# Optimization experiments

Hardware: AMD Instinct MI355X
Metric: run time of the kernel (lower is better)

The kernel has to match this reference:

```python
import jax, jax.numpy as jnp
import numpy as np

N_LEVELS = 16
BASE_RES = 16.0
MAX_RES = 128.0
LOG2_T = 19
T_SIZE = 2 ** LOG2_T
F = 2

# primes wrapped to int32 to mimic torch int32 overflow semantics
P0 = np.int32(1)
P1 = np.int32(np.uint32(2654435761))
P2 = np.int32(np.uint32(805459861))

# corner offsets matching (c_000,c_100,c_010,c_001,c_110,c_101,c_011,c_111)
OFFSETS = np.array([[0,0,0],[1,0,0],[0,1,0],[0,0,1],
                    [1,1,0],[1,0,1],[0,1,1],[1,1,1]], dtype=np.int32)


def setup_inputs() -> dict:
    key = jax.random.key(0)
    k1, k2 = jax.random.split(key)
    x = jax.random.uniform(k1, (1048576, 3), dtype=jnp.float32)
    hashtable = jax.random.uniform(k2, (T_SIZE, F), dtype=jnp.float32) * 2.0 - 1.0
    return {"x": x, "hashtable": hashtable}


def _resolutions():
    growth = np.exp((np.log(MAX_RES) - np.log(BASE_RES)) / (N_LEVELS - 1))
    return np.floor(BASE_RES * growth ** np.arange(N_LEVELS)).astype(np.float32)  # [L]


def reference(x, hashtable):
    res = jnp.asarray(_resolutions())                      # [L]
    xs = x[None, :, :] * res[:, None, None]                # [L,N,3]
    xf = jnp.floor(xs)
    xfi = xf.astype(jnp.int32)                             # [L,N,3]
    xci = jnp.ceil(xs).astype(jnp.int32)                   # [L,N,3]
    d = xs - xf                                            # [L,N,3] interp weights

    off = jnp.asarray(OFFSETS)[:, None, None, :]           # [8,1,1,3]
    corners = jnp.where(off == 1, xci[None], xfi[None])    # [8,L,N,3]

    h = (corners[..., 0] * P0) ^ (corners[..., 1] * P1) ^ (corners[..., 2] * P2)
    h = jnp.mod(h, T_SIZE)                                 # [8,L,N], nonnegative

    v = hashtable[h]                                       # [8,L,N,F]

    w = jnp.where(off == 1, d[None], 1.0 - d[None])        # [8,L,N,3]
    w = jnp.prod(w, axis=-1)                               # [8,L,N]

    enc = jnp.sum(v * w[..., None], axis=0)                # [L,N,F]
    N = x.shape[0]
    return jnp.transpose(enc, (1, 0, 2)).reshape(N, N_LEVELS * F)
```

## Files before the change

kernel.cpp:

```cpp
#include <hip/hip_runtime.h>


__constant__ float c_res[16] = {
    16.f, 18.f, 21.f, 24.f, 27.f, 32.f, 36.f, 42.f,
    48.f, 55.f, 64.f, 73.f, 84.f, 97.f, 111.f, 128.f
};

#define TMASK   0x7FFFFu
#define PRIME1  2654435761u
#define PRIME2  805459861u
#define NBUCKET 4096
#define CACHE_N 4467

__device__ __forceinline__ int bucket_of(float x0, float x1, float x2) {
    int c0 = (int)(x0 * 16.f); c0 = c0 < 0 ? 0 : (c0 > 15 ? 15 : c0);
    int c1 = (int)(x1 * 16.f); c1 = c1 < 0 ? 0 : (c1 > 15 ? 15 : c1);
    int c2 = (int)(x2 * 16.f); c2 = c2 < 0 ? 0 : (c2 > 15 ? 15 : c2);
    return (c0 << 8) | (c1 << 4) | c2;
}


__global__ __launch_bounds__(256)
void k_hist(const float* __restrict__ x, unsigned* __restrict__ cnt, int npts) {
    __shared__ unsigned h[NBUCKET];
    for (int i = threadIdx.x; i < NBUCKET; i += 256) h[i] = 0u;
    __syncthreads();
    int nb = gridDim.x;
    int chunk = (npts + nb - 1) / nb;
    int begin = blockIdx.x * chunk;
    int end   = begin + chunk; if (end > npts) end = npts;
    for (int i = begin + threadIdx.x; i < end; i += 256) {
        int b = bucket_of(x[3 * i], x[3 * i + 1], x[3 * i + 2]);
        atomicAdd(&h[b], 1u);
    }
    __syncthreads();
    for (int i = threadIdx.x; i < NBUCKET; i += 256)
        cnt[blockIdx.x * NBUCKET + i] = h[i];
}

template<int NBT>
__global__ __launch_bounds__(256)
void k_colscan(const unsigned* __restrict__ cnt, unsigned* __restrict__ base,
               unsigned* __restrict__ colsum) {
    const int RPG = NBT / 8;
    int col = blockIdx.x * 32 + (threadIdx.x & 31);
    int rg  = threadIdx.x >> 5;
    unsigned loc[RPG];
    unsigned s = 0;
    #pragma unroll
    for (int r = 0; r < RPG; ++r) {
        unsigned v = cnt[(size_t)(rg * RPG + r) * NBUCKET + col];
        loc[r] = s;
        s += v;
    }
    __shared__ unsigned t[8][32];
    t[rg][threadIdx.x & 31] = s;
    __syncthreads();
    unsigned pre = 0;
    for (int g = 0; g < rg; ++g) pre += t[g][threadIdx.x & 31];
    #pragma unroll
    for (int r = 0; r < RPG; ++r)
        base[(size_t)(rg * RPG + r) * NBUCKET + col] = pre + loc[r];
    if (rg == 7) colsum[col] = pre + s;
}

__global__ __launch_bounds__(1024)
void k_scan(const unsigned* __restrict__ colsum, unsigned* __restrict__ starts) {
    __shared__ unsigned tmp[1024];
    int t = threadIdx.x;
    unsigned v0 = colsum[4 * t + 0], v1 = colsum[4 * t + 1];
    unsigned v2 = colsum[4 * t + 2], v3 = colsum[4 * t + 3];
    unsigned s = v0 + v1 + v2 + v3;
    tmp[t] = s;
    __syncthreads();
    for (int off = 1; off < 1024; off <<= 1) {
        unsigned u = (t >= off) ? tmp[t - off] : 0u;
        __syncthreads();
        tmp[t] += u;
        __syncthreads();
    }
    unsigned excl = tmp[t] - s;
    starts[4 * t + 0] = excl;
    starts[4 * t + 1] = excl + v0;
    starts[4 * t + 2] = excl + v0 + v1;
    starts[4 * t + 3] = excl + v0 + v1 + v2;
    if (t == 1023) starts[4096] = tmp[1023];
}

template<int MODE>
__global__ __launch_bounds__(256)
void k_scatter(const float* __restrict__ x, const unsigned* __restrict__ base,
               const unsigned* __restrict__ starts, unsigned* __restrict__ perm,
               float4* __restrict__ xs, int npts) {
    __shared__ unsigned cur[NBUCKET];
    for (int i = threadIdx.x; i < NBUCKET; i += 256)
        cur[i] = starts[i] + base[blockIdx.x * NBUCKET + i];
    __syncthreads();
    int nb = gridDim.x;
    int chunk = (npts + nb - 1) / nb;
    int begin = blockIdx.x * chunk;
    int end   = begin + chunk; if (end > npts) end = npts;
    for (int i = begin + threadIdx.x; i < end; i += 256) {
        float x0 = x[3 * i], x1 = x[3 * i + 1], x2 = x[3 * i + 2];
        int b = bucket_of(x0, x1, x2);
        unsigned pos = atomicAdd(&cur[b], 1u);
        if constexpr (MODE == 0) {
            float4 v; v.x = x0; v.y = x1; v.z = x2;
            v.w = __uint_as_float((unsigned)i);
            xs[pos] = v;
        } else {
            perm[pos] = (unsigned)i;
        }
    }
}


template<int MODE>
__global__ __launch_bounds__(256)
void k_main(const float4* __restrict__ xs, const float* __restrict__ x,
            const unsigned* __restrict__ perm,
            const unsigned* __restrict__ starts, const float2* __restrict__ tab,
            float4* __restrict__ out4)
{
    __shared__ float2 cache[CACHE_N];
    __shared__ int4 metaA[16];
    __shared__ int4 metaB[16];

    int cell = blockIdx.x;
    int startp = starts[cell], endp = starts[cell + 1];
    if (startp == endp) return;

    int ci = (cell >> 8) & 15, cj = (cell >> 4) & 15, ck = cell & 15;
    float fi0 = ci * 0.0625f, fi1 = (ci + 1) * 0.0625f;
    float fj0 = cj * 0.0625f, fj1 = (cj + 1) * 0.0625f;
    float fk0 = ck * 0.0625f, fk1 = (ck + 1) * 0.0625f;

    int cbase = 0;
    #pragma unroll 1
    for (int l = 0; l < 16; ++l) {
        float r = c_res[l];
        int lo0 = (int)floorf(fi0 * r), hi0 = (int)ceilf(fi1 * r);
        int lo1 = (int)floorf(fj0 * r), hi1 = (int)ceilf(fj1 * r);
        int lo2 = (int)floorf(fk0 * r), hi2 = (int)ceilf(fk1 * r);
        int n0 = hi0 - lo0 + 1, n1 = hi1 - lo1 + 1, n2 = hi2 - lo2 + 1;
        int n12 = n1 * n2, tot = n0 * n12;
        for (int t = threadIdx.x; t < tot; t += 256) {
            int a = t / n12, rem = t - a * n12;
            int b = rem / n2, d = rem - b * n2;
            unsigned h = ((unsigned)(lo0 + a)
                        ^ ((unsigned)(lo1 + b) * PRIME1)
                        ^ ((unsigned)(lo2 + d) * PRIME2)) & TMASK;
            cache[cbase + t] = tab[h];
        }
        if (threadIdx.x == 0) {
            metaA[l] = make_int4(lo0, lo1, lo2, cbase);
            metaB[l] = make_int4(n12, n2, __float_as_int(r), 0);
        }
        cbase += tot;
    }
    __syncthreads();

    auto lvl = [&](int l, float a0, float a1, float a2, float& ex, float& ey) {
        int4 mA = metaA[l];
        int4 mB = metaB[l];
        float r = __int_as_float(mB.z);
        int n12 = mB.x, n2 = mB.y;
        float s0 = a0 * r, s1 = a1 * r, s2 = a2 * r;
        float f0 = floorf(s0), f1 = floorf(s1), f2 = floorf(s2);
        float d0 = s0 - f0, d1 = s1 - f1, d2 = s2 - f2;
        int A0 = (int)f0 - mA.x, A1 = (int)f1 - mA.y, A2 = (int)f2 - mA.z;
        int e0 = (d0 != 0.f) ? n12 : 0;
        int e1 = (d1 != 0.f) ? n2  : 0;
        int e2 = (d2 != 0.f) ? 1   : 0;
        int rA = mA.w + A0 * n12 + A1 * n2 + A2;

        float2 v0 = cache[rA];
        float2 v1 = cache[rA + e0];
        float2 v2 = cache[rA + e1];
        float2 v3 = cache[rA + e2];
        float2 v4 = cache[rA + e0 + e1];
        float2 v5 = cache[rA + e0 + e2];
        float2 v6 = cache[rA + e1 + e2];
        float2 v7 = cache[rA + e0 + e1 + e2];

        float u0 = 1.f - d0, u1 = 1.f - d1, u2 = 1.f - d2;
        float pa = u1 * u2, pb = d1 * u2, pc = u1 * d2, pe = d1 * d2;
        float w0 = u0 * pa, w1 = d0 * pa, w2 = u0 * pb, w3 = u0 * pc;
        float w4 = d0 * pb, w5 = d0 * pc, w6 = u0 * pe, w7 = d0 * pe;

        float rx = v0.x * w0, ry = v0.y * w0;
        rx += v1.x * w1;  ry += v1.y * w1;
        rx += v2.x * w2;  ry += v2.y * w2;
        rx += v3.x * w3;  ry += v3.y * w3;
        rx += v4.x * w4;  ry += v4.y * w4;
        rx += v5.x * w5;  ry += v5.y * w5;
        rx += v6.x * w6;  ry += v6.y * w6;
        rx += v7.x * w7;  ry += v7.y * w7;
        ex = rx; ey = ry;
    };

    auto fetch = [&](int s, float& a0, float& a1, float& a2, unsigned& pp) {
        if constexpr (MODE == 0) {
            float4 v = xs[s];
            a0 = v.x; a1 = v.y; a2 = v.z; pp = __float_as_uint(v.w);
        } else {
            pp = perm[s];
            a0 = x[3 * pp]; a1 = x[3 * pp + 1]; a2 = x[3 * pp + 2];
        }
    };

    int sp = startp + (int)threadIdx.x;
    if (sp >= endp) return;
    float x0, x1, x2; unsigned p;
    fetch(sp, x0, x1, x2, p);
    while (true) {
        int spn = sp + 256;
        bool more = spn < endp;
        float nx0, nx1, nx2; unsigned np;
        if (more) fetch(spn, nx0, nx1, nx2, np);

        #pragma unroll 1
        for (int lp = 0; lp < 8; ++lp) {
            float4 o;
            lvl(2 * lp,     x0, x1, x2, o.x, o.y);
            lvl(2 * lp + 1, x0, x1, x2, o.z, o.w);
            out4[(size_t)p * 8 + lp] = o;
        }

        if (!more) break;
        x0 = nx0; x1 = nx1; x2 = nx2; p = np;
        sp = spn;
    }
}

__global__ __launch_bounds__(256, 8)
void k_fallback(const float* __restrict__ x, const float2* __restrict__ tab,
                float2* __restrict__ out, int total) {
    int tid = blockIdx.x * 256 + threadIdx.x;
    if (tid >= total) return;
    int p = tid >> 4, l = tid & 15;
    float r = c_res[l];
    float s0 = x[3*p] * r, s1 = x[3*p+1] * r, s2 = x[3*p+2] * r;
    float f0 = floorf(s0), f1 = floorf(s1), f2 = floorf(s2);
    float d0 = s0 - f0, d1 = s1 - f1, d2 = s2 - f2;
    unsigned A0 = (unsigned)(int)f0, B0 = (unsigned)(int)ceilf(s0);
    unsigned A1 = (unsigned)(int)f1 * PRIME1, B1 = (unsigned)(int)ceilf(s1) * PRIME1;
    unsigned A2 = (unsigned)(int)f2 * PRIME2, B2 = (unsigned)(int)ceilf(s2) * PRIME2;
    unsigned h0=(A0^A1^A2)&TMASK, h1=(B0^A1^A2)&TMASK, h2=(A0^B1^A2)&TMASK;
    unsigned h3=(A0^A1^B2)&TMASK, h4=(B0^B1^A2)&TMASK, h5=(B0^A1^B2)&TMASK;
    unsigned h6=(A0^B1^B2)&TMASK, h7=(B0^B1^B2)&TMASK;
    float2 v0=tab[h0],v1=tab[h1],v2=tab[h2],v3=tab[h3];
    float2 v4=tab[h4],v5=tab[h5],v6=tab[h6],v7=tab[h7];
    float u0=1.f-d0,u1=1.f-d1,u2=1.f-d2;
    float ex = v0.x*(u0*u1*u2), ey = v0.y*(u0*u1*u2);
    ex += v1.x*(d0*u1*u2); ey += v1.y*(d0*u1*u2);
    ex += v2.x*(u0*d1*u2); ey += v2.y*(u0*d1*u2);
    ex += v3.x*(u0*u1*d2); ey += v3.y*(u0*u1*d2);
    ex += v4.x*(d0*d1*u2); ey += v4.y*(d0*d1*u2);
    ex += v5.x*(d0*u1*d2); ey += v5.y*(d0*u1*d2);
    ex += v6.x*(u0*d1*d2); ey += v6.y*(u0*d1*d2);
    ex += v7.x*(d0*d1*d2); ey += v7.y*(d0*d1*d2);
    float2 o; o.x = ex; o.y = ey; out[tid] = o;
}

extern "C" void kernel_launch(void* const* d_in, const int* in_sizes, int n_in,
                              void* d_out, int out_size, void* d_ws, size_t ws_size,
                              hipStream_t stream)
{
    const float*  x   = (const float*)d_in[0];
    const float2* tab = (const float2*)d_in[1];
    int npts = in_sizes[0] / 3;

    {
        const int NBA = 256;
        size_t off_cnt    = 0;
        size_t off_base   = off_cnt    + (size_t)NBA * NBUCKET * 4;
        size_t off_colsum = off_base   + (size_t)NBA * NBUCKET * 4;
        size_t off_starts = off_colsum + (size_t)NBUCKET * 4;
        size_t off_xs     = (off_starts + (size_t)(NBUCKET + 1) * 4 + 63)
                            & ~(size_t)63;
        size_t need       = off_xs + (size_t)npts * 16;
        if (ws_size >= need) {
            unsigned* cnt    = (unsigned*)((char*)d_ws + off_cnt);
            unsigned* base   = (unsigned*)((char*)d_ws + off_base);
            unsigned* colsum = (unsigned*)((char*)d_ws + off_colsum);
            unsigned* starts = (unsigned*)((char*)d_ws + off_starts);
            float4*   xs     = (float4*)  ((char*)d_ws + off_xs);

            k_hist        <<<NBA, 256, 0, stream>>>(x, cnt, npts);
            k_colscan<256><<<NBUCKET / 32, 256, 0, stream>>>(cnt, base, colsum);
            k_scan        <<<1, 1024, 0, stream>>>(colsum, starts);
            k_scatter<0>  <<<NBA, 256, 0, stream>>>(x, base, starts,
                                                    nullptr, xs, npts);
            k_main<0>     <<<NBUCKET, 256, 0, stream>>>(xs, x, nullptr, starts,
                                                        tab, (float4*)d_out);
            return;
        }
    }

    {
        const int NBB = 128;
        size_t off_cnt    = 0;
        size_t off_base   = off_cnt    + (size_t)NBB * NBUCKET * 4;
        size_t off_colsum = off_base   + (size_t)NBB * NBUCKET * 4;
        size_t off_starts = off_colsum + (size_t)NBUCKET * 4;
        size_t off_perm   = (off_starts + (size_t)(NBUCKET + 1) * 4 + 63)
                            & ~(size_t)63;
        size_t need       = off_perm + (size_t)npts * 4;
        if (ws_size >= need) {
            unsigned* cnt    = (unsigned*)((char*)d_ws + off_cnt);
            unsigned* base   = (unsigned*)((char*)d_ws + off_base);
            unsigned* colsum = (unsigned*)((char*)d_ws + off_colsum);
            unsigned* starts = (unsigned*)((char*)d_ws + off_starts);
            unsigned* perm   = (unsigned*)((char*)d_ws + off_perm);

            k_hist        <<<NBB, 256, 0, stream>>>(x, cnt, npts);
            k_colscan<128><<<NBUCKET / 32, 256, 0, stream>>>(cnt, base, colsum);
            k_scan        <<<1, 1024, 0, stream>>>(colsum, starts);
            k_scatter<1>  <<<NBB, 256, 0, stream>>>(x, base, starts,
                                                    perm, nullptr, npts);
            k_main<1>     <<<NBUCKET, 256, 0, stream>>>(nullptr, x, perm, starts,
                                                        tab, (float4*)d_out);
            return;
        }
    }

    int total = npts * 16;
    k_fallback<<<(total + 255) / 256, 256, 0, stream>>>(
        x, tab, (float2*)d_out, total);
}
```

Baseline: 257.9 us.

## Fuse binning passes into cooperative kernel and phase the per-cell table cache

Replaces the four binning kernels (histogram, column scan, scan, scatter) with one cooperative kernel that uses grid syncs and keeps each block's point chunk in LDS, so it reads x once and saves launches. The main kernel now fills its shared-memory corner cache in three level phases (14-15, 10-13, 0-9) instead of all 16 levels at once. This shrinks LDS from about 35KB to 14KB and adds a launch bound of 8 blocks per SM to raise occupancy. In exchange each point is re-read from xs three times, and there are extra barriers plus a fallback path if the cooperative launch fails.

Result: slower. 611.9 us (+137.3%).

```diff
diff --git a/kernel.cpp b/kernel.cpp
--- a/kernel.cpp
+++ b/kernel.cpp
@@ -1,4 +1,7 @@
 #include <hip/hip_runtime.h>
+#include <hip/hip_cooperative_groups.h>
+
+namespace cg = cooperative_groups;
 
 
 __constant__ float c_res[16] = {
@@ -10,13 +13,115 @@
 #define PRIME1  2654435761u
 #define PRIME2  805459861u
 #define NBUCKET 4096
-#define CACHE_N 4467
+#define CACHE_PH 1800
 
 __device__ __forceinline__ int bucket_of(float x0, float x1, float x2) {
     int c0 = (int)(x0 * 16.f); c0 = c0 < 0 ? 0 : (c0 > 15 ? 15 : c0);
     int c1 = (int)(x1 * 16.f); c1 = c1 < 0 ? 0 : (c1 > 15 ? 15 : c1);
     int c2 = (int)(x2 * 16.f); c2 = c2 < 0 ? 0 : (c2 > 15 ? 15 : c2);
     return (c0 << 8) | (c1 << 4) | c2;
+}
+
+__global__ __launch_bounds__(1024)
+void k_sort(const float* __restrict__ x, unsigned* __restrict__ cnt,
+            unsigned* __restrict__ base, unsigned* __restrict__ colsum,
+            unsigned* __restrict__ starts, float4* __restrict__ xs, int npts)
+{
+    extern __shared__ char smem[];
+    float*    xraw = (float*)smem;
+    unsigned* cur  = (unsigned*)(smem + 49152);
+    unsigned* tbl  = (unsigned*)(smem + 49152 + 16384);
+
+    const int tid = threadIdx.x;
+    const int blk = blockIdx.x;
+    const int chunk = npts >> 8;
+    const int begin = blk * chunk;
+
+    {
+        const float4* src = (const float4*)(x + (size_t)begin * 3);
+        float4* dst = (float4*)xraw;
+        const int nf4 = (chunk * 3) >> 2;
+        for (int i = tid; i < nf4; i += 1024) dst[i] = src[i];
+    }
+    for (int j = tid; j < NBUCKET; j += 1024) cur[j] = 0u;
+    __syncthreads();
+    for (int i = tid; i < chunk; i += 1024) {
+        int b = bucket_of(xraw[3*i], xraw[3*i+1], xraw[3*i+2]);
+        atomicAdd(&cur[b], 1u);
+    }
+    __syncthreads();
+    for (int j = tid; j < NBUCKET; j += 1024)
+        cnt[(size_t)blk * NBUCKET + j] = cur[j];
+
+    __threadfence();
+    cg::this_grid().sync();
+
+    {
+        int c = tid & 15, g = tid >> 4;
+        int col = blk * 16 + c;
+        unsigned loc[4], s = 0;
+        #pragma unroll
+        for (int k = 0; k < 4; ++k) {
+            unsigned v = cnt[(size_t)(g * 4 + k) * NBUCKET + col];
+            loc[k] = s; s += v;
+        }
+        tbl[g * 16 + c] = s;
+        __syncthreads();
+        for (int off = 1; off < 64; off <<= 1) {
+            unsigned u = (g >= off) ? tbl[(g - off) * 16 + c] : 0u;
+            __syncthreads();
+            tbl[g * 16 + c] += u;
+            __syncthreads();
+        }
+        unsigned pre = tbl[g * 16 + c] - s;
+        #pragma unroll
+        for (int k = 0; k < 4; ++k)
+            base[(size_t)(g * 4 + k) * NBUCKET + col] = pre + loc[k];
+        if (g == 63) colsum[col] = pre + s;
+    }
+
+    __threadfence();
+    cg::this_grid().sync();
+
+    {
+        unsigned v0 = colsum[4*tid+0], v1 = colsum[4*tid+1];
+        unsigned v2 = colsum[4*tid+2], v3 = colsum[4*tid+3];
+        unsigned s = v0 + v1 + v2 + v3;
+        tbl[tid] = s;
+        __syncthreads();
+        for (int off = 1; off < 1024; off <<= 1) {
+            unsigned u = (tid >= off) ? tbl[tid - off] : 0u;
+            __syncthreads();
+            tbl[tid] += u;
+            __syncthreads();
+        }
+        unsigned excl = tbl[tid] - s;
+        unsigned b0 = base[(size_t)blk * NBUCKET + 4*tid + 0];
+        unsigned b1 = base[(size_t)blk * NBUCKET + 4*tid + 1];
+        unsigned b2 = base[(size_t)blk * NBUCKET + 4*tid + 2];
+        unsigned b3 = base[(size_t)blk * NBUCKET + 4*tid + 3];
+        cur[4*tid+0] = excl + b0;
+        cur[4*tid+1] = excl + v0 + b1;
+        cur[4*tid+2] = excl + v0 + v1 + b2;
+        cur[4*tid+3] = excl + v0 + v1 + v2 + b3;
+        if (blk == 0) {
+            starts[4*tid+0] = excl;
+            starts[4*tid+1] = excl + v0;
+            starts[4*tid+2] = excl + v0 + v1;
+            starts[4*tid+3] = excl + v0 + v1 + v2;
+            if (tid == 1023) starts[NBUCKET] = tbl[1023];
+        }
+    }
+    __syncthreads();
+
+    for (int i = tid; i < chunk; i += 1024) {
+        float x0 = xraw[3*i], x1 = xraw[3*i+1], x2 = xraw[3*i+2];
+        int b = bucket_of(x0, x1, x2);
+        unsigned pos = atomicAdd(&cur[b], 1u);
+        float4 v; v.x = x0; v.y = x1; v.z = x2;
+        v.w = __uint_as_float((unsigned)(begin + i));
+        xs[pos] = v;
+    }
 }
 
 
@@ -116,13 +221,13 @@
 
 
 template<int MODE>
-__global__ __launch_bounds__(256)
+__global__ __launch_bounds__(256, 8)
 void k_main(const float4* __restrict__ xs, const float* __restrict__ x,
             const unsigned* __restrict__ perm,
             const unsigned* __restrict__ starts, const float2* __restrict__ tab,
             float4* __restrict__ out4)
 {
-    __shared__ float2 cache[CACHE_N];
+    __shared__ float2 cache[CACHE_PH];
     __shared__ int4 metaA[16];
     __shared__ int4 metaB[16];
 
@@ -134,31 +239,6 @@
     float fi0 = ci * 0.0625f, fi1 = (ci + 1) * 0.0625f;
     float fj0 = cj * 0.0625f, fj1 = (cj + 1) * 0.0625f;
     float fk0 = ck * 0.0625f, fk1 = (ck + 1) * 0.0625f;
-
-    int cbase = 0;
-    #pragma unroll 1
-    for (int l = 0; l < 16; ++l) {
-        float r = c_res[l];
-        int lo0 = (int)floorf(fi0 * r), hi0 = (int)ceilf(fi1 * r);
-        int lo1 = (int)floorf(fj0 * r), hi1 = (int)ceilf(fj1 * r);
-        int lo2 = (int)floorf(fk0 * r), hi2 = (int)ceilf(fk1 * r);
-        int n0 = hi0 - lo0 + 1, n1 = hi1 - lo1 + 1, n2 = hi2 - lo2 + 1;
-        int n12 = n1 * n2, tot = n0 * n12;
-        for (int t = threadIdx.x; t < tot; t += 256) {
-            int a = t / n12, rem = t - a * n12;
-            int b = rem / n2, d = rem - b * n2;
-            unsigned h = ((unsigned)(lo0 + a)
-                        ^ ((unsigned)(lo1 + b) * PRIME1)
-                        ^ ((unsigned)(lo2 + d) * PRIME2)) & TMASK;
-            cache[cbase + t] = tab[h];
-        }
-        if (threadIdx.x == 0) {
-            metaA[l] = make_int4(lo0, lo1, lo2, cbase);
-            metaB[l] = make_int4(n12, n2, __float_as_int(r), 0);
-        }
-        cbase += tot;
-    }
-    __syncthreads();
 
     auto lvl = [&](int l, float a0, float a1, float a2, float& ex, float& ey) {
         int4 mA = metaA[l];
@@ -199,37 +279,54 @@
         ex = rx; ey = ry;
     };
 
-    auto fetch = [&](int s, float& a0, float& a1, float& a2, unsigned& pp) {
-        if constexpr (MODE == 0) {
-            float4 v = xs[s];
-            a0 = v.x; a1 = v.y; a2 = v.z; pp = __float_as_uint(v.w);
-        } else {
-            pp = perm[s];
-            a0 = x[3 * pp]; a1 = x[3 * pp + 1]; a2 = x[3 * pp + 2];
-        }
-    };
-
-    int sp = startp + (int)threadIdx.x;
-    if (sp >= endp) return;
-    float x0, x1, x2; unsigned p;
-    fetch(sp, x0, x1, x2, p);
-    while (true) {
-        int spn = sp + 256;
-        bool more = spn < endp;
-        float nx0, nx1, nx2; unsigned np;
-        if (more) fetch(spn, nx0, nx1, nx2, np);
-
+    #pragma unroll
+    for (int ph = 0; ph < 3; ++ph) {
+        const int llo = (ph == 0) ? 14 : (ph == 1) ? 10 : 0;
+        const int lhi = (ph == 0) ? 16 : (ph == 1) ? 14 : 10;
+
+        int cbase = 0;
         #pragma unroll 1
-        for (int lp = 0; lp < 8; ++lp) {
-            float4 o;
-            lvl(2 * lp,     x0, x1, x2, o.x, o.y);
-            lvl(2 * lp + 1, x0, x1, x2, o.z, o.w);
-            out4[(size_t)p * 8 + lp] = o;
-        }
-
-        if (!more) break;
-        x0 = nx0; x1 = nx1; x2 = nx2; p = np;
-        sp = spn;
+        for (int l = llo; l < lhi; ++l) {
+            float r = c_res[l];
+            int lo0 = (int)floorf(fi0 * r), hi0 = (int)ceilf(fi1 * r);
+            int lo1 = (int)floorf(fj0 * r), hi1 = (int)ceilf(fj1 * r);
+            int lo2 = (int)floorf(fk0 * r), hi2 = (int)ceilf(fk1 * r);
+            int n0 = hi0 - lo0 + 1, n1 = hi1 - lo1 + 1, n2 = hi2 - lo2 + 1;
+            int n12 = n1 * n2, tot = n0 * n12;
+            for (int t = threadIdx.x; t < tot; t += 256) {
+                int a = t / n12, rem = t - a * n12;
+                int b = rem / n2, d = rem - b * n2;
+                unsigned h = ((unsigned)(lo0 + a)
+                            ^ ((unsigned)(lo1 + b) * PRIME1)
+                            ^ ((unsigned)(lo2 + d) * PRIME2)) & TMASK;
+                cache[cbase + t] = tab[h];
+            }
+            if (threadIdx.x == 0) {
+                metaA[l] = make_int4(lo0, lo1, lo2, cbase);
+                metaB[l] = make_int4(n12, n2, __float_as_int(r), 0);
+            }
+            cbase += tot;
+        }
+        __syncthreads();
+
+        for (int sp = startp + (int)threadIdx.x; sp < endp; sp += 256) {
+            float x0, x1, x2; unsigned p;
+            if constexpr (MODE == 0) {
+                float4 v = xs[sp];
+                x0 = v.x; x1 = v.y; x2 = v.z; p = __float_as_uint(v.w);
+            } else {
+                p = perm[sp];
+                x0 = x[3 * p]; x1 = x[3 * p + 1]; x2 = x[3 * p + 2];
+            }
+            #pragma unroll 1
+            for (int lp = (llo >> 1); lp < (lhi >> 1); ++lp) {
+                float4 o;
+                lvl(2 * lp,     x0, x1, x2, o.x, o.y);
+                lvl(2 * lp + 1, x0, x1, x2, o.z, o.w);
+                out4[(size_t)p * 8 + lp] = o;
+            }
+        }
+        __syncthreads();
     }
 }
 
@@ -287,11 +384,24 @@
             unsigned* starts = (unsigned*)((char*)d_ws + off_starts);
             float4*   xs     = (float4*)  ((char*)d_ws + off_xs);
 
-            k_hist        <<<NBA, 256, 0, stream>>>(x, cnt, npts);
-            k_colscan<256><<<NBUCKET / 32, 256, 0, stream>>>(cnt, base, colsum);
-            k_scan        <<<1, 1024, 0, stream>>>(colsum, starts);
-            k_scatter<0>  <<<NBA, 256, 0, stream>>>(x, base, starts,
-                                                    nullptr, xs, npts);
+            bool coop_ok = false;
+            if ((npts % 1024) == 0 && (npts >> 8) <= 4096) {
+                int np = npts;
+                void* args[] = { (void*)&x, (void*)&cnt, (void*)&base,
+                                 (void*)&colsum, (void*)&starts, (void*)&xs,
+                                 (void*)&np };
+                unsigned shmem = 49152u + 16384u + 4096u;
+                hipError_t e = hipLaunchCooperativeKernel(
+                    (void*)k_sort, dim3(256), dim3(1024), args, shmem, stream);
+                coop_ok = (e == hipSuccess);
+            }
+            if (!coop_ok) {
+                k_hist        <<<NBA, 256, 0, stream>>>(x, cnt, npts);
+                k_colscan<256><<<NBUCKET / 32, 256, 0, stream>>>(cnt, base, colsum);
+                k_scan        <<<1, 1024, 0, stream>>>(colsum, starts);
+                k_scatter<0>  <<<NBA, 256, 0, stream>>>(x, base, starts,
+                                                        nullptr, xs, npts);
+            }
             k_main<0>     <<<NBUCKET, 256, 0, stream>>>(xs, x, nullptr, starts,
                                                         tab, (float4*)d_out);
             return;
```

## Replace per-block count/colscan sort with global atomic histogram and cursors

Applied to the files above, without the earlier changes.

The binning pipeline drops the per-block count matrix and column-scan kernel. It now uses a global histogram built with shared atomics then global atomic merges, a single scan that also initialises global cursors, and a scatter using global atomics on those cursors. The main kernel moves to 512 threads per block with an 8-block occupancy hint and drops the software prefetch of the next point. This cuts launches and the workspace traffic of the count and base matrices, but adds heavy global-atomic contention in the scatter and makes the sort order nondeterministic.

Result: slower. 311.0 us (+20.6%).

```diff
diff --git a/kernel.cpp b/kernel.cpp
--- a/kernel.cpp
+++ b/kernel.cpp
@@ -19,57 +19,30 @@
     return (c0 << 8) | (c1 << 4) | c2;
 }
 
-
 __global__ __launch_bounds__(256)
-void k_hist(const float* __restrict__ x, unsigned* __restrict__ cnt, int npts) {
+void k_hist(const float* __restrict__ x, unsigned* __restrict__ hist, int npts) {
     __shared__ unsigned h[NBUCKET];
-    for (int i = threadIdx.x; i < NBUCKET; i += 256) h[i] = 0u;
-    __syncthreads();
-    int nb = gridDim.x;
-    int chunk = (npts + nb - 1) / nb;
-    int begin = blockIdx.x * chunk;
-    int end   = begin + chunk; if (end > npts) end = npts;
-    for (int i = begin + threadIdx.x; i < end; i += 256) {
+    for (int j = threadIdx.x; j < NBUCKET; j += 256) h[j] = 0u;
+    __syncthreads();
+    int stride = gridDim.x * 256;
+    for (int i = blockIdx.x * 256 + threadIdx.x; i < npts; i += stride) {
         int b = bucket_of(x[3 * i], x[3 * i + 1], x[3 * i + 2]);
         atomicAdd(&h[b], 1u);
     }
     __syncthreads();
-    for (int i = threadIdx.x; i < NBUCKET; i += 256)
-        cnt[blockIdx.x * NBUCKET + i] = h[i];
-}
-
-template<int NBT>
-__global__ __launch_bounds__(256)
-void k_colscan(const unsigned* __restrict__ cnt, unsigned* __restrict__ base,
-               unsigned* __restrict__ colsum) {
-    const int RPG = NBT / 8;
-    int col = blockIdx.x * 32 + (threadIdx.x & 31);
-    int rg  = threadIdx.x >> 5;
-    unsigned loc[RPG];
-    unsigned s = 0;
-    #pragma unroll
-    for (int r = 0; r < RPG; ++r) {
-        unsigned v = cnt[(size_t)(rg * RPG + r) * NBUCKET + col];
-        loc[r] = s;
-        s += v;
-    }
-    __shared__ unsigned t[8][32];
-    t[rg][threadIdx.x & 31] = s;
-    __syncthreads();
-    unsigned pre = 0;
-    for (int g = 0; g < rg; ++g) pre += t[g][threadIdx.x & 31];
-    #pragma unroll
-    for (int r = 0; r < RPG; ++r)
-        base[(size_t)(rg * RPG + r) * NBUCKET + col] = pre + loc[r];
-    if (rg == 7) colsum[col] = pre + s;
+    for (int j = threadIdx.x; j < NBUCKET; j += 256) {
+        unsigned v = h[j];
+        if (v) atomicAdd(&hist[j], v);
+    }
 }
 
 __global__ __launch_bounds__(1024)
-void k_scan(const unsigned* __restrict__ colsum, unsigned* __restrict__ starts) {
+void k_scan(const unsigned* __restrict__ hist, unsigned* __restrict__ starts,
+            unsigned* __restrict__ cursor) {
     __shared__ unsigned tmp[1024];
     int t = threadIdx.x;
-    unsigned v0 = colsum[4 * t + 0], v1 = colsum[4 * t + 1];
-    unsigned v2 = colsum[4 * t + 2], v3 = colsum[4 * t + 3];
+    unsigned v0 = hist[4 * t + 0], v1 = hist[4 * t + 1];
+    unsigned v2 = hist[4 * t + 2], v3 = hist[4 * t + 3];
     unsigned s = v0 + v1 + v2 + v3;
     tmp[t] = s;
     __syncthreads();
@@ -80,30 +53,23 @@
         __syncthreads();
     }
     unsigned excl = tmp[t] - s;
-    starts[4 * t + 0] = excl;
-    starts[4 * t + 1] = excl + v0;
-    starts[4 * t + 2] = excl + v0 + v1;
-    starts[4 * t + 3] = excl + v0 + v1 + v2;
-    if (t == 1023) starts[4096] = tmp[1023];
+    unsigned s1 = excl + v0, s2 = s1 + v1, s3 = s2 + v2;
+    starts[4 * t + 0] = excl;  cursor[4 * t + 0] = excl;
+    starts[4 * t + 1] = s1;    cursor[4 * t + 1] = s1;
+    starts[4 * t + 2] = s2;    cursor[4 * t + 2] = s2;
+    starts[4 * t + 3] = s3;    cursor[4 * t + 3] = s3;
+    if (t == 1023) starts[NBUCKET] = tmp[1023];
 }
 
 template<int MODE>
 __global__ __launch_bounds__(256)
-void k_scatter(const float* __restrict__ x, const unsigned* __restrict__ base,
-               const unsigned* __restrict__ starts, unsigned* __restrict__ perm,
-               float4* __restrict__ xs, int npts) {
-    __shared__ unsigned cur[NBUCKET];
-    for (int i = threadIdx.x; i < NBUCKET; i += 256)
-        cur[i] = starts[i] + base[blockIdx.x * NBUCKET + i];
-    __syncthreads();
-    int nb = gridDim.x;
-    int chunk = (npts + nb - 1) / nb;
-    int begin = blockIdx.x * chunk;
-    int end   = begin + chunk; if (end > npts) end = npts;
-    for (int i = begin + threadIdx.x; i < end; i += 256) {
+void k_scatter(const float* __restrict__ x, unsigned* __restrict__ cursor,
+               unsigned* __restrict__ perm, float4* __restrict__ xs, int npts) {
+    int stride = gridDim.x * 256;
+    for (int i = blockIdx.x * 256 + threadIdx.x; i < npts; i += stride) {
         float x0 = x[3 * i], x1 = x[3 * i + 1], x2 = x[3 * i + 2];
         int b = bucket_of(x0, x1, x2);
-        unsigned pos = atomicAdd(&cur[b], 1u);
+        unsigned pos = atomicAdd(&cursor[b], 1u);
         if constexpr (MODE == 0) {
             float4 v; v.x = x0; v.y = x1; v.z = x2;
             v.w = __uint_as_float((unsigned)i);
@@ -116,7 +82,7 @@
 
 
 template<int MODE>
-__global__ __launch_bounds__(256)
+__global__ __launch_bounds__(512, 8)
 void k_main(const float4* __restrict__ xs, const float* __restrict__ x,
             const unsigned* __restrict__ perm,
             const unsigned* __restrict__ starts, const float2* __restrict__ tab,
@@ -144,7 +110,7 @@
         int lo2 = (int)floorf(fk0 * r), hi2 = (int)ceilf(fk1 * r);
         int n0 = hi0 - lo0 + 1, n1 = hi1 - lo1 + 1, n2 = hi2 - lo2 + 1;
         int n12 = n1 * n2, tot = n0 * n12;
-        for (int t = threadIdx.x; t < tot; t += 256) {
+        for (int t = threadIdx.x; t < tot; t += 512) {
             int a = t / n12, rem = t - a * n12;
             int b = rem / n2, d = rem - b * n2;
             unsigned h = ((unsigned)(lo0 + a)
@@ -199,26 +165,15 @@
         ex = rx; ey = ry;
     };
 
-    auto fetch = [&](int s, float& a0, float& a1, float& a2, unsigned& pp) {
+    for (int sp = startp + (int)threadIdx.x; sp < endp; sp += 512) {
+        float x0, x1, x2; unsigned p;
         if constexpr (MODE == 0) {
-            float4 v = xs[s];
-            a0 = v.x; a1 = v.y; a2 = v.z; pp = __float_as_uint(v.w);
+            float4 v = xs[sp];
+            x0 = v.x; x1 = v.y; x2 = v.z; p = __float_as_uint(v.w);
         } else {
-            pp = perm[s];
-            a0 = x[3 * pp]; a1 = x[3 * pp + 1]; a2 = x[3 * pp + 2];
-        }
-    };
-
-    int sp = startp + (int)threadIdx.x;
-    if (sp >= endp) return;
-    float x0, x1, x2; unsigned p;
-    fetch(sp, x0, x1, x2, p);
-    while (true) {
-        int spn = sp + 256;
-        bool more = spn < endp;
-        float nx0, nx1, nx2; unsigned np;
-        if (more) fetch(spn, nx0, nx1, nx2, np);
-
+            p = perm[sp];
+            x0 = x[3 * p]; x1 = x[3 * p + 1]; x2 = x[3 * p + 2];
+        }
         #pragma unroll 1
         for (int lp = 0; lp < 8; ++lp) {
             float4 o;
@@ -226,10 +181,6 @@
             lvl(2 * lp + 1, x0, x1, x2, o.z, o.w);
             out4[(size_t)p * 8 + lp] = o;
         }
-
-        if (!more) break;
-        x0 = nx0; x1 = nx1; x2 = nx2; p = np;
-        sp = spn;
     }
 }
 
@@ -271,56 +222,43 @@
     const float2* tab = (const float2*)d_in[1];
     int npts = in_sizes[0] / 3;
 
+    size_t off_hist   = 0;
+    size_t off_starts = off_hist + (size_t)NBUCKET * 4;
+    size_t off_cursor = (off_starts + (size_t)(NBUCKET + 1) * 4 + 63) & ~(size_t)63;
+    size_t off_pay    = (off_cursor + (size_t)NBUCKET * 4 + 63) & ~(size_t)63;
+
     {
-        const int NBA = 256;
-        size_t off_cnt    = 0;
-        size_t off_base   = off_cnt    + (size_t)NBA * NBUCKET * 4;
-        size_t off_colsum = off_base   + (size_t)NBA * NBUCKET * 4;
-        size_t off_starts = off_colsum + (size_t)NBUCKET * 4;
-        size_t off_xs     = (off_starts + (size_t)(NBUCKET + 1) * 4 + 63)
-                            & ~(size_t)63;
-        size_t need       = off_xs + (size_t)npts * 16;
+        size_t need = off_pay + (size_t)npts * 16;
         if (ws_size >= need) {
-            unsigned* cnt    = (unsigned*)((char*)d_ws + off_cnt);
-            unsigned* base   = (unsigned*)((char*)d_ws + off_base);
-            unsigned* colsum = (unsigned*)((char*)d_ws + off_colsum);
+            unsigned* hist   = (unsigned*)((char*)d_ws + off_hist);
             unsigned* starts = (unsigned*)((char*)d_ws + off_starts);
-            float4*   xs     = (float4*)  ((char*)d_ws + off_xs);
-
-            k_hist        <<<NBA, 256, 0, stream>>>(x, cnt, npts);
-            k_colscan<256><<<NBUCKET / 32, 256, 0, stream>>>(cnt, base, colsum);
-            k_scan        <<<1, 1024, 0, stream>>>(colsum, starts);
-            k_scatter<0>  <<<NBA, 256, 0, stream>>>(x, base, starts,
-                                                    nullptr, xs, npts);
-            k_main<0>     <<<NBUCKET, 256, 0, stream>>>(xs, x, nullptr, starts,
-                                                        tab, (float4*)d_out);
+            unsigned* cursor = (unsigned*)((char*)d_ws + off_cursor);
+            float4*   xs     = (float4*)  ((char*)d_ws + off_pay);
+
+            hipMemsetAsync(hist, 0, (size_t)NBUCKET * 4, stream);
+            k_hist      <<<256, 256, 0, stream>>>(x, hist, npts);
+            k_scan      <<<1, 1024, 0, stream>>>(hist, starts, cursor);
+            k_scatter<0><<<2048, 256, 0, stream>>>(x, cursor, nullptr, xs, npts);
+            k_main<0>   <<<NBUCKET, 512, 0, stream>>>(xs, x, nullptr, starts,
+                                                      tab, (float4*)d_out);
             return;
         }
     }
 
     {
-        const int NBB = 128;
-        size_t off_cnt    = 0;
-        size_t off_base   = off_cnt    + (size_t)NBB * NBUCKET * 4;
-        size_t off_colsum = off_base   + (size_t)NBB * NBUCKET * 4;
-        size_t off_starts = off_colsum + (size_t)NBUCKET * 4;
-        size_t off_perm   = (off_starts + (size_t)(NBUCKET + 1) * 4 + 63)
-                            & ~(size_t)63;
-        size_t need       = off_perm + (size_t)npts * 4;
+        size_t need = off_pay + (size_t)npts * 4;
         if (ws_size >= need) {
-            unsigned* cnt    = (unsigned*)((char*)d_ws + off_cnt);
-            unsigned* base   = (unsigned*)((char*)d_ws + off_base);
-            unsigned* colsum = (unsigned*)((char*)d_ws + off_colsum);
+            unsigned* hist   = (unsigned*)((char*)d_ws + off_hist);
             unsigned* starts = (unsigned*)((char*)d_ws + off_starts);
-            unsigned* perm   = (unsigned*)((char*)d_ws + off_perm);
-
-            k_hist        <<<NBB, 256, 0, stream>>>(x, cnt, npts);
-            k_colscan<128><<<NBUCKET / 32, 256, 0, stream>>>(cnt, base, colsum);
-            k_scan        <<<1, 1024, 0, stream>>>(colsum, starts);
-            k_scatter<1>  <<<NBB, 256, 0, stream>>>(x, base, starts,
-                                                    perm, nullptr, npts);
-            k_main<1>     <<<NBUCKET, 256, 0, stream>>>(nullptr, x, perm, starts,
-                                                        tab, (float4*)d_out);
+            unsigned* cursor = (unsigned*)((char*)d_ws + off_cursor);
+            unsigned* perm   = (unsigned*)((char*)d_ws + off_pay);
+
+            hipMemsetAsync(hist, 0, (size_t)NBUCKET * 4, stream);
+            k_hist      <<<256, 256, 0, stream>>>(x, hist, npts);
+            k_scan      <<<1, 1024, 0, stream>>>(hist, starts, cursor);
+            k_scatter<1><<<2048, 256, 0, stream>>>(x, cursor, perm, nullptr, npts);
+            k_main<1>   <<<NBUCKET, 512, 0, stream>>>(nullptr, x, perm, starts,
+                                                      tab, (float4*)d_out);
             return;
         }
     }
```

## Widen blocks, pair adjacent cache loads, drop software prefetch in main kernel

Applied to the files above, without the earlier changes.

Histogram and scatter kernels now run 1024 threads per block, and the main kernel runs 512 threads with a launch bound asking for 8 waves per SIMD. The z-neighbour corner loads become paired loads at index and index+1, selected by whether the z fraction is nonzero, so the addresses are independent of that predicate; the cache gets one padding element to keep the +1 read in bounds. The manual next-point prefetch loop is replaced by a plain strided loop to lower register pressure. The fallback path with fewer blocks now uses 256 blocks, which raises its workspace need, and the larger main-kernel blocks add more idle threads in sparse cells.

Result: slower. 278.7 us (+8.1%).

```diff
diff --git a/kernel.cpp b/kernel.cpp
--- a/kernel.cpp
+++ b/kernel.cpp
@@ -10,6 +10,7 @@
 #define PRIME1  2654435761u
 #define PRIME2  805459861u
 #define NBUCKET 4096
+#define NB      256
 #define CACHE_N 4467
 
 __device__ __forceinline__ int bucket_of(float x0, float x1, float x2) {
@@ -20,29 +21,27 @@
 }
 
 
-__global__ __launch_bounds__(256)
+__global__ __launch_bounds__(1024)
 void k_hist(const float* __restrict__ x, unsigned* __restrict__ cnt, int npts) {
     __shared__ unsigned h[NBUCKET];
-    for (int i = threadIdx.x; i < NBUCKET; i += 256) h[i] = 0u;
-    __syncthreads();
-    int nb = gridDim.x;
-    int chunk = (npts + nb - 1) / nb;
+    for (int i = threadIdx.x; i < NBUCKET; i += 1024) h[i] = 0u;
+    __syncthreads();
+    int chunk = (npts + NB - 1) / NB;
     int begin = blockIdx.x * chunk;
     int end   = begin + chunk; if (end > npts) end = npts;
-    for (int i = begin + threadIdx.x; i < end; i += 256) {
+    for (int i = begin + threadIdx.x; i < end; i += 1024) {
         int b = bucket_of(x[3 * i], x[3 * i + 1], x[3 * i + 2]);
         atomicAdd(&h[b], 1u);
     }
     __syncthreads();
-    for (int i = threadIdx.x; i < NBUCKET; i += 256)
+    for (int i = threadIdx.x; i < NBUCKET; i += 1024)
         cnt[blockIdx.x * NBUCKET + i] = h[i];
 }
 
-template<int NBT>
 __global__ __launch_bounds__(256)
 void k_colscan(const unsigned* __restrict__ cnt, unsigned* __restrict__ base,
                unsigned* __restrict__ colsum) {
-    const int RPG = NBT / 8;
+    const int RPG = NB / 8;
     int col = blockIdx.x * 32 + (threadIdx.x & 31);
     int rg  = threadIdx.x >> 5;
     unsigned loc[RPG];
@@ -88,19 +87,18 @@
 }
 
 template<int MODE>
-__global__ __launch_bounds__(256)
+__global__ __launch_bounds__(1024)
 void k_scatter(const float* __restrict__ x, const unsigned* __restrict__ base,
                const unsigned* __restrict__ starts, unsigned* __restrict__ perm,
                float4* __restrict__ xs, int npts) {
     __shared__ unsigned cur[NBUCKET];
-    for (int i = threadIdx.x; i < NBUCKET; i += 256)
+    for (int i = threadIdx.x; i < NBUCKET; i += 1024)
         cur[i] = starts[i] + base[blockIdx.x * NBUCKET + i];
     __syncthreads();
-    int nb = gridDim.x;
-    int chunk = (npts + nb - 1) / nb;
+    int chunk = (npts + NB - 1) / NB;
     int begin = blockIdx.x * chunk;
     int end   = begin + chunk; if (end > npts) end = npts;
-    for (int i = begin + threadIdx.x; i < end; i += 256) {
+    for (int i = begin + threadIdx.x; i < end; i += 1024) {
         float x0 = x[3 * i], x1 = x[3 * i + 1], x2 = x[3 * i + 2];
         int b = bucket_of(x0, x1, x2);
         unsigned pos = atomicAdd(&cur[b], 1u);
@@ -116,13 +114,13 @@
 
 
 template<int MODE>
-__global__ __launch_bounds__(256)
+__global__ __launch_bounds__(512, 8)
 void k_main(const float4* __restrict__ xs, const float* __restrict__ x,
             const unsigned* __restrict__ perm,
             const unsigned* __restrict__ starts, const float2* __restrict__ tab,
             float4* __restrict__ out4)
 {
-    __shared__ float2 cache[CACHE_N];
+    __shared__ float2 cache[CACHE_N + 1];
     __shared__ int4 metaA[16];
     __shared__ int4 metaB[16];
 
@@ -144,7 +142,7 @@
         int lo2 = (int)floorf(fk0 * r), hi2 = (int)ceilf(fk1 * r);
         int n0 = hi0 - lo0 + 1, n1 = hi1 - lo1 + 1, n2 = hi2 - lo2 + 1;
         int n12 = n1 * n2, tot = n0 * n12;
-        for (int t = threadIdx.x; t < tot; t += 256) {
+        for (int t = threadIdx.x; t < tot; t += 512) {
             int a = t / n12, rem = t - a * n12;
             int b = rem / n2, d = rem - b * n2;
             unsigned h = ((unsigned)(lo0 + a)
@@ -171,17 +169,22 @@
         int A0 = (int)f0 - mA.x, A1 = (int)f1 - mA.y, A2 = (int)f2 - mA.z;
         int e0 = (d0 != 0.f) ? n12 : 0;
         int e1 = (d1 != 0.f) ? n2  : 0;
-        int e2 = (d2 != 0.f) ? 1   : 0;
+        bool e2 = (d2 != 0.f);
         int rA = mA.w + A0 * n12 + A1 * n2 + A2;
-
-        float2 v0 = cache[rA];
-        float2 v1 = cache[rA + e0];
-        float2 v2 = cache[rA + e1];
-        float2 v3 = cache[rA + e2];
-        float2 v4 = cache[rA + e0 + e1];
-        float2 v5 = cache[rA + e0 + e2];
-        float2 v6 = cache[rA + e1 + e2];
-        float2 v7 = cache[rA + e0 + e1 + e2];
+        int rB = rA + e1, rC = rA + e0, rD = rA + e0 + e1;
+
+        float2 pa0 = cache[rA], pa1 = cache[rA + 1];
+        float2 pb0 = cache[rB], pb1 = cache[rB + 1];
+        float2 pc0 = cache[rC], pc1 = cache[rC + 1];
+        float2 pd0 = cache[rD], pd1 = cache[rD + 1];
+        float2 v0 = pa0;
+        float2 v3 = e2 ? pa1 : pa0;
+        float2 v2 = pb0;
+        float2 v6 = e2 ? pb1 : pb0;
+        float2 v1 = pc0;
+        float2 v5 = e2 ? pc1 : pc0;
+        float2 v4 = pd0;
+        float2 v7 = e2 ? pd1 : pd0;
 
         float u0 = 1.f - d0, u1 = 1.f - d1, u2 = 1.f - d2;
         float pa = u1 * u2, pb = d1 * u2, pc = u1 * d2, pe = d1 * d2;
@@ -199,26 +202,15 @@
         ex = rx; ey = ry;
     };
 
-    auto fetch = [&](int s, float& a0, float& a1, float& a2, unsigned& pp) {
+    for (int sp = startp + (int)threadIdx.x; sp < endp; sp += 512) {
+        float x0, x1, x2; unsigned p;
         if constexpr (MODE == 0) {
-            float4 v = xs[s];
-            a0 = v.x; a1 = v.y; a2 = v.z; pp = __float_as_uint(v.w);
+            float4 v = xs[sp];
+            x0 = v.x; x1 = v.y; x2 = v.z; p = __float_as_uint(v.w);
         } else {
-            pp = perm[s];
-            a0 = x[3 * pp]; a1 = x[3 * pp + 1]; a2 = x[3 * pp + 2];
-        }
-    };
-
-    int sp = startp + (int)threadIdx.x;
-    if (sp >= endp) return;
-    float x0, x1, x2; unsigned p;
-    fetch(sp, x0, x1, x2, p);
-    while (true) {
-        int spn = sp + 256;
-        bool more = spn < endp;
-        float nx0, nx1, nx2; unsigned np;
-        if (more) fetch(spn, nx0, nx1, nx2, np);
-
+            p = perm[sp];
+            x0 = x[3 * p]; x1 = x[3 * p + 1]; x2 = x[3 * p + 2];
+        }
         #pragma unroll 1
         for (int lp = 0; lp < 8; ++lp) {
             float4 o;
@@ -226,10 +218,6 @@
             lvl(2 * lp + 1, x0, x1, x2, o.z, o.w);
             out4[(size_t)p * 8 + lp] = o;
         }
-
-        if (!more) break;
-        x0 = nx0; x1 = nx1; x2 = nx2; p = np;
-        sp = spn;
     }
 }
 
@@ -271,56 +259,49 @@
     const float2* tab = (const float2*)d_in[1];
     int npts = in_sizes[0] / 3;
 
+    size_t off_cnt    = 0;
+    size_t off_base   = off_cnt    + (size_t)NB * NBUCKET * 4;
+    size_t off_colsum = off_base   + (size_t)NB * NBUCKET * 4;
+    size_t off_starts = off_colsum + (size_t)NBUCKET * 4;
+    size_t off_pay    = (off_starts + (size_t)(NBUCKET + 1) * 4 + 63)
+                        & ~(size_t)63;
+
     {
-        const int NBA = 256;
-        size_t off_cnt    = 0;
-        size_t off_base   = off_cnt    + (size_t)NBA * NBUCKET * 4;
-        size_t off_colsum = off_base   + (size_t)NBA * NBUCKET * 4;
-        size_t off_starts = off_colsum + (size_t)NBUCKET * 4;
-        size_t off_xs     = (off_starts + (size_t)(NBUCKET + 1) * 4 + 63)
-                            & ~(size_t)63;
-        size_t need       = off_xs + (size_t)npts * 16;
+        size_t need = off_pay + (size_t)npts * 16;
         if (ws_size >= need) {
             unsigned* cnt    = (unsigned*)((char*)d_ws + off_cnt);
             unsigned* base   = (unsigned*)((char*)d_ws + off_base);
             unsigned* colsum = (unsigned*)((char*)d_ws + off_colsum);
             unsigned* starts = (unsigned*)((char*)d_ws + off_starts);
-            float4*   xs     = (float4*)  ((char*)d_ws + off_xs);
-
-            k_hist        <<<NBA, 256, 0, stream>>>(x, cnt, npts);
-            k_colscan<256><<<NBUCKET / 32, 256, 0, stream>>>(cnt, base, colsum);
-            k_scan        <<<1, 1024, 0, stream>>>(colsum, starts);
-            k_scatter<0>  <<<NBA, 256, 0, stream>>>(x, base, starts,
-                                                    nullptr, xs, npts);
-            k_main<0>     <<<NBUCKET, 256, 0, stream>>>(xs, x, nullptr, starts,
-                                                        tab, (float4*)d_out);
+            float4*   xs     = (float4*)  ((char*)d_ws + off_pay);
+
+            k_hist      <<<NB, 1024, 0, stream>>>(x, cnt, npts);
+            k_colscan   <<<NBUCKET / 32, 256, 0, stream>>>(cnt, base, colsum);
+            k_scan      <<<1, 1024, 0, stream>>>(colsum, starts);
+            k_scatter<0><<<NB, 1024, 0, stream>>>(x, base, starts,
+                                                  nullptr, xs, npts);
+            k_main<0>   <<<NBUCKET, 512, 0, stream>>>(xs, x, nullptr, starts,
+                                                      tab, (float4*)d_out);
             return;
         }
     }
 
     {
-        const int NBB = 128;
-        size_t off_cnt    = 0;
-        size_t off_base   = off_cnt    + (size_t)NBB * NBUCKET * 4;
-        size_t off_colsum = off_base   + (size_t)NBB * NBUCKET * 4;
-        size_t off_starts = off_colsum + (size_t)NBUCKET * 4;
-        size_t off_perm   = (off_starts + (size_t)(NBUCKET + 1) * 4 + 63)
-                            & ~(size_t)63;
-        size_t need       = off_perm + (size_t)npts * 4;
+        size_t need = off_pay + (size_t)npts * 4;
         if (ws_size >= need) {
             unsigned* cnt    = (unsigned*)((char*)d_ws + off_cnt);
             unsigned* base   = (unsigned*)((char*)d_ws + off_base);
             unsigned* colsum = (unsigned*)((char*)d_ws + off_colsum);
             unsigned* starts = (unsigned*)((char*)d_ws + off_starts);
-            unsigned* perm   = (unsigned*)((char*)d_ws + off_perm);
-
-            k_hist        <<<NBB, 256, 0, stream>>>(x, cnt, npts);
-            k_colscan<128><<<NBUCKET / 32, 256, 0, stream>>>(cnt, base, colsum);
-            k_scan        <<<1, 1024, 0, stream>>>(colsum, starts);
-            k_scatter<1>  <<<NBB, 256, 0, stream>>>(x, base, starts,
-                                                    perm, nullptr, npts);
-            k_main<1>     <<<NBUCKET, 256, 0, stream>>>(nullptr, x, perm, starts,
-                                                        tab, (float4*)d_out);
+            unsigned* perm   = (unsigned*)((char*)d_ws + off_pay);
+
+            k_hist      <<<NB, 1024, 0, stream>>>(x, cnt, npts);
+            k_colscan   <<<NBUCKET / 32, 256, 0, stream>>>(cnt, base, colsum);
+            k_scan      <<<1, 1024, 0, stream>>>(colsum, starts);
+            k_scatter<1><<<NB, 1024, 0, stream>>>(x, base, starts,
+                                                  perm, nullptr, npts);
+            k_main<1>   <<<NBUCKET, 512, 0, stream>>>(nullptr, x, perm, starts,
+                                                      tab, (float4*)d_out);
             return;
         }
     }
```
